# Performance work log

Measured on AMD Instinct MI355X. Metric: run time of the kernel, lower is better.

The kernel has to match this reference:

```python
import jax, jax.numpy as jnp
import numpy as np

N_NODES = 100000
N_EDGES = 1600000
NUM_FEATURES = 128
HIDDEN = 128


def _linear_init(key, fan_in, fan_out):
    kw, kb = jax.random.split(key)
    bound = 1.0 / np.sqrt(fan_in)
    w = jax.random.uniform(kw, (fan_in, fan_out), jnp.float32, -bound, bound)
    b = jax.random.uniform(kb, (fan_out,), jnp.float32, -bound, bound)
    return w, b


def setup_inputs() -> dict:
    key = jax.random.key(0)
    ks = jax.random.split(key, 8)
    x = jax.random.normal(ks[0], (N_NODES, NUM_FEATURES), jnp.float32)
    edge_index = jax.random.randint(ks[1], (2, N_EDGES), 0, N_NODES, jnp.int64)
    w11, b11 = _linear_init(ks[2], NUM_FEATURES, HIDDEN)
    w12, b12 = _linear_init(ks[3], HIDDEN, HIDDEN)
    w21, b21 = _linear_init(ks[4], HIDDEN, HIDDEN)
    w22, b22 = _linear_init(ks[5], HIDDEN, HIDDEN)
    w31, b31 = _linear_init(ks[6], HIDDEN, HIDDEN)
    w32, b32 = _linear_init(ks[7], HIDDEN, 1)
    return {"x": x, "edge_index": edge_index,
            "w11": w11, "b11": b11, "w12": w12, "b12": b12,
            "w21": w21, "b21": b21, "w22": w22, "b22": b22,
            "w31": w31, "b31": b31, "w32": w32, "b32": b32}


def _gin_conv(x, src, dst, w1, b1, w2, b2):
    # GINConv (eps=0): h_i = MLP(x_i + sum_{j->i} x_j)
    agg = jax.ops.segment_sum(x[src], dst, num_segments=N_NODES)
    h = x + agg
    h = jax.nn.relu(h @ w1 + b1)
    return h @ w2 + b2


def reference(x, edge_index, w11, b11, w12, b12, w21, b21, w22, b22, w31, b31, w32, b32):
    src, dst = edge_index[0], edge_index[1]
    h = _gin_conv(x, src, dst, w11, b11, w12, b12)
    h = _gin_conv(h, src, dst, w21, b21, w22, b22)
    h = _gin_conv(h, src, dst, w31, b31, w32, b32)  # [N, 1]
    return h
```

## Files before the change

### kernel.cpp

```cpp
#include <hip/hip_runtime.h>

#define NN 100000
#define NE 1600000
#define F 128
#define NBUCK ((NN + 255) >> 8)
#define EPB (NE / 256)

typedef _Float16 f16x8 __attribute__((ext_vector_type(8)));
typedef float    f32x4 __attribute__((ext_vector_type(4)));
typedef unsigned short ushort8v __attribute__((ext_vector_type(8)));
typedef unsigned short ushort4v __attribute__((ext_vector_type(4)));

__device__ inline unsigned short f2h(float f) {
    _Float16 h = (_Float16)f;
    return __builtin_bit_cast(unsigned short, h);
}
__device__ inline float h2f(unsigned short u) {
    return (float)__builtin_bit_cast(_Float16, u);
}

__global__ __launch_bounds__(256) void k_bhist(const int* __restrict__ dst, int* __restrict__ bcnt) {
    __shared__ int sc[NBUCK];
    for (int i = threadIdx.x; i < NBUCK; i += 256) sc[i] = 0;
    __syncthreads();
    int stride = gridDim.x * 256;
    for (int e = blockIdx.x * 256 + threadIdx.x; e < NE; e += stride)
        atomicAdd(&sc[dst[e] >> 8], 1);
    __syncthreads();
    for (int i = threadIdx.x; i < NBUCK; i += 256) {
        int c = sc[i];
        if (c) atomicAdd(&bcnt[i], c);
    }
}

__global__ void k_bscan(const int* __restrict__ bcnt, int* __restrict__ bbase, int* __restrict__ bcur) {
    __shared__ int s[512];
    int t = threadIdx.x;
    int v = (t < NBUCK) ? bcnt[t] : 0;
    s[t] = v;
    __syncthreads();
    for (int off = 1; off < 512; off <<= 1) {
        int u = (t >= off) ? s[t - off] : 0;
        __syncthreads();
        s[t] += u;
        __syncthreads();
    }
    int excl = s[t] - v;
    if (t < NBUCK) { bbase[t] = excl; bcur[t] = excl; }
    if (t == 0) bbase[NBUCK] = NE;
}

__global__ __launch_bounds__(256) void k_scatterA(const int* __restrict__ src,
                                                  const int* __restrict__ dst,
                                                  int* __restrict__ bcur,
                                                  unsigned* __restrict__ scratch) {
    __shared__ uint2 sEdge[EPB];
    __shared__ int cnt[512];
    __shared__ int scn[512];
    __shared__ int cntB[512];
    __shared__ int gbase[512];
    __shared__ int ssum[256];

    const int tid = threadIdx.x;
    const int ebase = blockIdx.x * EPB;

#pragma unroll
    for (int i = tid; i < 512; i += 256) { cnt[i] = 0; cntB[i] = 0; }
    __syncthreads();

    for (int i = tid; i < EPB; i += 256) {
        int b = dst[ebase + i] >> 8;
        atomicAdd(&cnt[b], 1);
    }
    __syncthreads();

    int c0 = cnt[2 * tid], c1 = cnt[2 * tid + 1];
    ssum[tid] = c0 + c1;
    __syncthreads();
    for (int off = 1; off < 256; off <<= 1) {
        int v = (tid >= off) ? ssum[tid - off] : 0;
        __syncthreads();
        ssum[tid] += v;
        __syncthreads();
    }
    int texcl = (tid == 0) ? 0 : ssum[tid - 1];
    scn[2 * tid] = texcl;
    scn[2 * tid + 1] = texcl + c0;
#pragma unroll
    for (int i = tid; i < NBUCK; i += 256) {
        int c = cnt[i];
        gbase[i] = c ? atomicAdd(&bcur[i], c) : 0;
    }
    __syncthreads();

    for (int i = tid; i < EPB; i += 256) {
        int s = src[ebase + i], d = dst[ebase + i];
        int b = d >> 8;
        int rank = atomicAdd(&cntB[b], 1);
        sEdge[scn[b] + rank] = make_uint2((unsigned)s, (unsigned)d);
    }
    __syncthreads();

    for (int i = tid; i < EPB; i += 256) {
        uint2 ed = sEdge[i];
        int b = (int)(ed.y >> 8);
        unsigned w = ((ed.y & 255u) << 24) | ed.x;
        scratch[gbase[b] + (i - scn[b])] = w;
    }
}

__global__ __launch_bounds__(256) void k_fillB(const int* __restrict__ bbase,
                                               const unsigned* __restrict__ scratch,
                                               int* __restrict__ row_ptr,
                                               int* __restrict__ csr) {
    __shared__ int cnt[256];
    __shared__ int s[256];
    __shared__ int cur[256];
    int b = blockIdx.x;
    int base = bbase[b], end = bbase[b + 1];
    int t = threadIdx.x;
    cnt[t] = 0;
    __syncthreads();
    for (int i = base + t; i < end; i += 256)
        atomicAdd(&cnt[scratch[i] >> 24], 1);
    __syncthreads();
    int v = cnt[t];
    s[t] = v;
    __syncthreads();
    for (int off = 1; off < 256; off <<= 1) {
        int u = (t >= off) ? s[t - off] : 0;
        __syncthreads();
        s[t] += u;
        __syncthreads();
    }
    int excl = s[t] - v;
    int node = (b << 8) + t;
    if (node < NN) row_ptr[node] = base + excl;
    if (b == NBUCK - 1 && t == 0) row_ptr[NN] = NE;
    cur[t] = excl;
    __syncthreads();
    for (int i = base + t; i < end; i += 256) {
        unsigned w = scratch[i];
        int n = w >> 24;
        int p = atomicAdd(&cur[n], 1);
        csr[base + p] = (int)(w & 0xFFFFFFu);
    }
}

__global__ void k_x2h(const float* __restrict__ x, unsigned short* __restrict__ xh) {
    int idx = blockIdx.x * 256 + threadIdx.x;
    float4 v = ((const float4*)x)[idx];
    ushort4v h;
    h.x = f2h(v.x);
    h.y = f2h(v.y);
    h.z = f2h(v.z);
    h.w = f2h(v.w);
    ((ushort4v*)xh)[idx] = h;
}

struct WPack {
    const float* w[5];
    unsigned short* t[5];
};

__global__ void k_w2h(WPack p) {
    int which = blockIdx.x >> 6;
    int idx = (blockIdx.x & 63) * 256 + threadIdx.x;
    int n = idx >> 7, k = idx & 127;
    p.t[which][idx] = f2h(p.w[which][k * 128 + n]);
}

__global__ __launch_bounds__(256) void k_agg(const unsigned short* __restrict__ h,
                                             const int* __restrict__ row_ptr,
                                             const int* __restrict__ csr,
                                             unsigned short* __restrict__ u) {
    int g   = threadIdx.x >> 4;
    int l16 = threadIdx.x & 15;
    int node = blockIdx.x * 16 + g;
    int lofs = l16 * 8;
    size_t base = (size_t)node * F + lofs;
    ushort8v sh = *(const ushort8v*)&h[base];
    float a[8];
#pragma unroll
    for (int k = 0; k < 8; ++k) a[k] = h2f(sh[k]);
    int s = row_ptr[node], e = row_ptr[node + 1];
    int p = s;
    for (; p + 8 <= e; p += 8) {
        ushort8v v[8];
#pragma unroll
        for (int q = 0; q < 8; ++q) {
            int j = csr[p + q];
            v[q] = *(const ushort8v*)&h[(size_t)j * F + lofs];
        }
#pragma unroll
        for (int k = 0; k < 8; ++k) {
            float t0 = (h2f(v[0][k]) + h2f(v[1][k])) + (h2f(v[2][k]) + h2f(v[3][k]));
            float t1 = (h2f(v[4][k]) + h2f(v[5][k])) + (h2f(v[6][k]) + h2f(v[7][k]));
            a[k] += t0 + t1;
        }
    }
    if (p + 4 <= e) {
        ushort8v v[4];
#pragma unroll
        for (int q = 0; q < 4; ++q) {
            int j = csr[p + q];
            v[q] = *(const ushort8v*)&h[(size_t)j * F + lofs];
        }
#pragma unroll
        for (int k = 0; k < 8; ++k)
            a[k] += (h2f(v[0][k]) + h2f(v[1][k])) + (h2f(v[2][k]) + h2f(v[3][k]));
        p += 4;
    }
    if (p + 2 <= e) {
        int j0 = csr[p], j1 = csr[p + 1];
        ushort8v v0 = *(const ushort8v*)&h[(size_t)j0 * F + lofs];
        ushort8v v1 = *(const ushort8v*)&h[(size_t)j1 * F + lofs];
#pragma unroll
        for (int k = 0; k < 8; ++k) a[k] += h2f(v0[k]) + h2f(v1[k]);
        p += 2;
    }
    if (p < e) {
        int j0 = csr[p];
        ushort8v v0 = *(const ushort8v*)&h[(size_t)j0 * F + lofs];
#pragma unroll
        for (int k = 0; k < 8; ++k) a[k] += h2f(v0[k]);
    }
    ushort8v o;
#pragma unroll
    for (int k = 0; k < 8; ++k) o[k] = f2h(a[k]);
    *(ushort8v*)&u[base] = o;
}

template <int L3>
__global__ __launch_bounds__(256, 6) void k_mlp(const unsigned short* __restrict__ A,
                                                const unsigned short* __restrict__ W1,
                                                const float* __restrict__ b1,
                                                const unsigned short* __restrict__ W2,
                                                const float* __restrict__ b2,
                                                const float* __restrict__ w32,
                                                const float* __restrict__ b32,
                                                unsigned short* __restrict__ H,
                                                float* __restrict__ out) {
    __shared__ __align__(16) unsigned short sA[64 * 128];

    const int tid = threadIdx.x;
    const int row0 = blockIdx.x * 64;
    const int cg   = tid >> 6;
    const int lane = tid & 63;
    const int m16  = lane & 15;
    const int quad = lane >> 4;

    {
        const ushort8v* g = (const ushort8v*)(A + (size_t)row0 * F);
#pragma unroll
        for (int i = 0; i < 4; ++i) {
            int fg = i * 256 + tid;
            int r = fg >> 4, u = fg & 15;
            ushort8v v = {};
            if (row0 + r < NN) v = g[fg];
            *(ushort8v*)&sA[r * 128 + ((u ^ (r & 15)) << 3)] = v;
        }
    }
    __syncthreads();

    f32x4 acc[4][2] = {};
#pragma unroll
    for (int ks = 0; ks < 4; ++ks) {
        f16x8 a[4];
#pragma unroll
        for (int rt = 0; rt < 4; ++rt) {
            int rowL = rt * 16 + m16;
            int u = ks * 4 + quad;
            a[rt] = *(const f16x8*)&sA[rowL * 128 + ((u ^ (rowL & 15)) << 3)];
        }
#pragma unroll
        for (int ct = 0; ct < 2; ++ct) {
            int widx = (cg * 32 + ct * 16 + m16) * 128 + ks * 32 + quad * 8;
            f16x8 b = *(const f16x8*)&W1[widx];
#pragma unroll
            for (int rt = 0; rt < 4; ++rt)
                acc[rt][ct] = __builtin_amdgcn_mfma_f32_16x16x32_f16(a[rt], b, acc[rt][ct], 0, 0, 0);
        }
    }

    if (L3) {
        float* psf = (float*)sA;
        __syncthreads();
#pragma unroll
        for (int rt = 0; rt < 4; ++rt) {
            float s[4] = {0.f, 0.f, 0.f, 0.f};
#pragma unroll
            for (int ct = 0; ct < 2; ++ct) {
                int col = cg * 32 + ct * 16 + m16;
                float bv = b1[col];
                float wv = w32[col];
#pragma unroll
                for (int i = 0; i < 4; ++i) {
                    float v = fmaxf(acc[rt][ct][i] + bv, 0.f);
                    s[i] += v * wv;
                }
            }
#pragma unroll
            for (int i = 0; i < 4; ++i) {
#pragma unroll
                for (int mask = 1; mask < 16; mask <<= 1)
                    s[i] += __shfl_xor(s[i], mask, 64);
            }
            if (m16 == 0) {
#pragma unroll
                for (int i = 0; i < 4; ++i) {
                    int rowL = rt * 16 + quad * 4 + i;
                    psf[rowL * 4 + cg] = s[i];
                }
            }
        }
        __syncthreads();
        if (tid < 64) {
            int row = row0 + tid;
            if (row < NN)
                out[row] = (psf[tid * 4] + psf[tid * 4 + 1]) + (psf[tid * 4 + 2] + psf[tid * 4 + 3]) + b32[0];
        }
        return;
    }

    __syncthreads();
#pragma unroll
    for (int rt = 0; rt < 4; ++rt) {
#pragma unroll
        for (int ct = 0; ct < 2; ++ct) {
            int col = cg * 32 + ct * 16 + m16;
            float bv = b1[col];
#pragma unroll
            for (int i = 0; i < 4; ++i) {
                int rL = rt * 16 + quad * 4 + i;
                float v = fmaxf(acc[rt][ct][i] + bv, 0.f);
                sA[rL * 128 + (((col >> 3) ^ (rL & 15)) << 3) + (col & 7)] = f2h(v);
            }
        }
    }
    __syncthreads();

    f32x4 acc2[4][2] = {};
#pragma unroll
    for (int ks = 0; ks < 4; ++ks) {
        f16x8 a[4];
#pragma unroll
        for (int rt = 0; rt < 4; ++rt) {
            int rowL = rt * 16 + m16;
            int u = ks * 4 + quad;
            a[rt] = *(const f16x8*)&sA[rowL * 128 + ((u ^ (rowL & 15)) << 3)];
        }
#pragma unroll
        for (int ct = 0; ct < 2; ++ct) {
            int widx = (cg * 32 + ct * 16 + m16) * 128 + ks * 32 + quad * 8;
            f16x8 b = *(const f16x8*)&W2[widx];
#pragma unroll
            for (int rt = 0; rt < 4; ++rt)
                acc2[rt][ct] = __builtin_amdgcn_mfma_f32_16x16x32_f16(a[rt], b, acc2[rt][ct], 0, 0, 0);
        }
    }

    __syncthreads();
#pragma unroll
    for (int rt = 0; rt < 4; ++rt) {
#pragma unroll
        for (int ct = 0; ct < 2; ++ct) {
            int col = cg * 32 + ct * 16 + m16;
            float bv = b2[col];
#pragma unroll
            for (int i = 0; i < 4; ++i) {
                int rL = rt * 16 + quad * 4 + i;
                float v = acc2[rt][ct][i] + bv;
                sA[rL * 128 + (((col >> 3) ^ (rL & 15)) << 3) + (col & 7)] = f2h(v);
            }
        }
    }
    __syncthreads();
    {
        ushort8v* go = (ushort8v*)(H + (size_t)row0 * F);
#pragma unroll
        for (int i = 0; i < 4; ++i) {
            int fg = i * 256 + tid;
            int r = fg >> 4, u = fg & 15;
            if (row0 + r < NN)
                go[fg] = *(const ushort8v*)&sA[r * 128 + ((u ^ (r & 15)) << 3)];
        }
    }
}

static inline size_t align256(size_t x) { return (x + 255) & ~(size_t)255; }

extern "C" void kernel_launch(void* const* d_in, const int* in_sizes, int n_in,
                              void* d_out, int out_size, void* d_ws, size_t ws_size,
                              hipStream_t stream) {
    const float* x   = (const float*)d_in[0];
    const int*   ei  = (const int*)d_in[1];
    const float* w11 = (const float*)d_in[2];
    const float* b11 = (const float*)d_in[3];
    const float* w12 = (const float*)d_in[4];
    const float* b12 = (const float*)d_in[5];
    const float* w21 = (const float*)d_in[6];
    const float* b21 = (const float*)d_in[7];
    const float* w22 = (const float*)d_in[8];
    const float* b22 = (const float*)d_in[9];
    const float* w31 = (const float*)d_in[10];
    const float* b31 = (const float*)d_in[11];
    const float* w32 = (const float*)d_in[12];
    const float* b32 = (const float*)d_in[13];
    float* out = (float*)d_out;

    const int* src = ei;
    const int* dst = ei + NE;

    char* ws = (char*)d_ws;
    size_t off = 0;
    unsigned short* Abuf = (unsigned short*)(ws + off); off += align256((size_t)NN * F * 2);
    unsigned short* Bbuf = (unsigned short*)(ws + off); off += align256((size_t)NN * F * 2);
    int* bcnt    = (int*)(ws + off); off += align256((size_t)NBUCK * 4);
    int* bbase   = (int*)(ws + off); off += align256((size_t)(NBUCK + 1) * 4);
    int* bcur    = (int*)(ws + off); off += align256((size_t)NBUCK * 4);
    int* row_ptr = (int*)(ws + off); off += align256((size_t)(NN + 1) * 4);
    int* csr     = (int*)(ws + off); off += align256((size_t)NE * 4);
    unsigned* scratch = (unsigned*)(ws + off); off += align256((size_t)NE * 4);
    unsigned short* wt[5];
    for (int i = 0; i < 5; ++i) {
        wt[i] = (unsigned short*)(ws + off); off += align256((size_t)128 * 128 * 2);
    }
    (void)ws_size;

    WPack wp;
    wp.w[0] = w11; wp.w[1] = w12; wp.w[2] = w21; wp.w[3] = w22; wp.w[4] = w31;
    for (int i = 0; i < 5; ++i) wp.t[i] = wt[i];
    k_w2h<<<320, 256, 0, stream>>>(wp);
    k_x2h<<<(NN * F / 4 + 255) / 256, 256, 0, stream>>>(x, Abuf);

    (void)hipMemsetAsync(bcnt, 0, (size_t)NBUCK * 4, stream);
    k_bhist<<<256, 256, 0, stream>>>(dst, bcnt);
    k_bscan<<<1, 512, 0, stream>>>(bcnt, bbase, bcur);
    k_scatterA<<<256, 256, 0, stream>>>(src, dst, bcur, scratch);
    k_fillB<<<NBUCK, 256, 0, stream>>>(bbase, scratch, row_ptr, csr);

    const int aggBlocks = NN / 16;
    const int mlpBlocks = (NN + 63) / 64;

    k_agg<<<aggBlocks, 256, 0, stream>>>(Abuf, row_ptr, csr, Bbuf);
    k_mlp<0><<<mlpBlocks, 256, 0, stream>>>(Bbuf, wt[0], b11, wt[1], b12,
                                            nullptr, nullptr, Abuf, nullptr);
    k_agg<<<aggBlocks, 256, 0, stream>>>(Abuf, row_ptr, csr, Bbuf);
    k_mlp<0><<<mlpBlocks, 256, 0, stream>>>(Bbuf, wt[2], b21, wt[3], b22,
                                            nullptr, nullptr, Abuf, nullptr);
    k_agg<<<aggBlocks, 256, 0, stream>>>(Abuf, row_ptr, csr, Bbuf);
    k_mlp<1><<<mlpBlocks, 256, 0, stream>>>(Bbuf, wt[4], b31, nullptr, nullptr,
                                            w32, b32, nullptr, out);
}
```

Baseline: 442.2 us.

## Slice node features into 8 column planes for cache-local aggregation

Stores the fp16 feature matrices as 8 planes of 16 columns each (32 bytes per node per plane) instead of row-major 256-byte rows. Aggregation blocks each work on one plane for 128 nodes, so the gather working set per plane (about 3.2 MB) can stay resident in L2/LLC while random neighbor rows are fetched. The conversion and MLP load/store paths are rewritten to read and write the planar layout. The cost is smaller 32-byte gather segments per edge and more strided MLP loads and stores.

```diff
diff --git a/kernel.cpp b/kernel.cpp
--- a/kernel.cpp
+++ b/kernel.cpp
@@ -5,6 +5,7 @@
 #define F 128
 #define NBUCK ((NN + 255) >> 8)
 #define EPB (NE / 256)
+#define PL ((size_t)NN * 16)
 
 typedef _Float16 f16x8 __attribute__((ext_vector_type(8)));
 typedef float    f32x4 __attribute__((ext_vector_type(4)));
@@ -148,14 +149,15 @@
 }
 
 __global__ void k_x2h(const float* __restrict__ x, unsigned short* __restrict__ xh) {
-    int idx = blockIdx.x * 256 + threadIdx.x;
-    float4 v = ((const float4*)x)[idx];
-    ushort4v h;
-    h.x = f2h(v.x);
-    h.y = f2h(v.y);
-    h.z = f2h(v.z);
-    h.w = f2h(v.w);
-    ((ushort4v*)xh)[idx] = h;
+    int i = blockIdx.x * 256 + threadIdx.x;
+    int n = i >> 4, g = i & 15;
+    int s = g >> 1, hh = g & 1;
+    const float4* src = (const float4*)(x + (size_t)n * F + g * 8);
+    float4 v0 = src[0], v1 = src[1];
+    ushort8v o;
+    o[0] = f2h(v0.x); o[1] = f2h(v0.y); o[2] = f2h(v0.z); o[3] = f2h(v0.w);
+    o[4] = f2h(v1.x); o[5] = f2h(v1.y); o[6] = f2h(v1.z); o[7] = f2h(v1.w);
+    *(ushort8v*)&xh[(size_t)s * PL + (size_t)n * 16 + hh * 8] = o;
 }
 
 struct WPack {
@@ -174,23 +176,28 @@
                                              const int* __restrict__ row_ptr,
                                              const int* __restrict__ csr,
                                              unsigned short* __restrict__ u) {
-    int g   = threadIdx.x >> 4;
-    int l16 = threadIdx.x & 15;
-    int node = blockIdx.x * 16 + g;
-    int lofs = l16 * 8;
-    size_t base = (size_t)node * F + lofs;
-    ushort8v sh = *(const ushort8v*)&h[base];
+    const int s  = blockIdx.x & 7;
+    const int nb = blockIdx.x >> 3;
+    const int rl = threadIdx.x >> 1;
+    const int hh = threadIdx.x & 1;
+    const int node = nb * 128 + rl;
+    if (node >= NN) return;
+    const unsigned short* P = h + (size_t)s * PL;
+    unsigned short* Q = u + (size_t)s * PL;
+    const size_t base = (size_t)node * 16 + hh * 8;
+    ushort8v sh = *(const ushort8v*)&P[base];
     float a[8];
 #pragma unroll
     for (int k = 0; k < 8; ++k) a[k] = h2f(sh[k]);
-    int s = row_ptr[node], e = row_ptr[node + 1];
-    int p = s;
+    int st = row_ptr[node], e = row_ptr[node + 1];
+    int p = st;
+    const int ho = hh * 8;
     for (; p + 8 <= e; p += 8) {
         ushort8v v[8];
 #pragma unroll
         for (int q = 0; q < 8; ++q) {
             int j = csr[p + q];
-            v[q] = *(const ushort8v*)&h[(size_t)j * F + lofs];
+            v[q] = *(const ushort8v*)&P[(size_t)j * 16 + ho];
         }
 #pragma unroll
         for (int k = 0; k < 8; ++k) {
@@ -204,7 +211,7 @@
 #pragma unroll
         for (int q = 0; q < 4; ++q) {
             int j = csr[p + q];
-            v[q] = *(const ushort8v*)&h[(size_t)j * F + lofs];
+            v[q] = *(const ushort8v*)&P[(size_t)j * 16 + ho];
         }
 #pragma unroll
         for (int k = 0; k < 8; ++k)
@@ -213,22 +220,22 @@
     }
     if (p + 2 <= e) {
         int j0 = csr[p], j1 = csr[p + 1];
-        ushort8v v0 = *(const ushort8v*)&h[(size_t)j0 * F + lofs];
-        ushort8v v1 = *(const ushort8v*)&h[(size_t)j1 * F + lofs];
+        ushort8v v0 = *(const ushort8v*)&P[(size_t)j0 * 16 + ho];
+        ushort8v v1 = *(const ushort8v*)&P[(size_t)j1 * 16 + ho];
 #pragma unroll
         for (int k = 0; k < 8; ++k) a[k] += h2f(v0[k]) + h2f(v1[k]);
         p += 2;
     }
     if (p < e) {
         int j0 = csr[p];
-        ushort8v v0 = *(const ushort8v*)&h[(size_t)j0 * F + lofs];
+        ushort8v v0 = *(const ushort8v*)&P[(size_t)j0 * 16 + ho];
 #pragma unroll
         for (int k = 0; k < 8; ++k) a[k] += h2f(v0[k]);
     }
     ushort8v o;
 #pragma unroll
     for (int k = 0; k < 8; ++k) o[k] = f2h(a[k]);
-    *(ushort8v*)&u[base] = o;
+    *(ushort8v*)&Q[base] = o;
 }
 
 template <int L3>
@@ -250,16 +257,20 @@
     const int m16  = lane & 15;
     const int quad = lane >> 4;
 
-    {
-        const ushort8v* g = (const ushort8v*)(A + (size_t)row0 * F);
-#pragma unroll
-        for (int i = 0; i < 4; ++i) {
-            int fg = i * 256 + tid;
-            int r = fg >> 4, u = fg & 15;
-            ushort8v v = {};
-            if (row0 + r < NN) v = g[fg];
-            *(ushort8v*)&sA[r * 128 + ((u ^ (r & 15)) << 3)] = v;
-        }
+#pragma unroll
+    for (int it = 0; it < 2; ++it) {
+        int unit = it * 256 + tid;
+        int s = unit >> 6, r = unit & 63;
+        int node = row0 + r;
+        ushort8v v0 = {}, v1 = {};
+        if (node < NN) {
+            const unsigned short* P = A + (size_t)s * PL + (size_t)node * 16;
+            v0 = *(const ushort8v*)&P[0];
+            v1 = *(const ushort8v*)&P[8];
+        }
+        int u0 = 2 * s, u1 = 2 * s + 1;
+        *(ushort8v*)&sA[r * 128 + ((u0 ^ (r & 15)) << 3)] = v0;
+        *(ushort8v*)&sA[r * 128 + ((u1 ^ (r & 15)) << 3)] = v1;
     }
     __syncthreads();
 
@@ -376,14 +387,18 @@
         }
     }
     __syncthreads();
-    {
-        ushort8v* go = (ushort8v*)(H + (size_t)row0 * F);
-#pragma unroll
-        for (int i = 0; i < 4; ++i) {
-            int fg = i * 256 + tid;
-            int r = fg >> 4, u = fg & 15;
-            if (row0 + r < NN)
-                go[fg] = *(const ushort8v*)&sA[r * 128 + ((u ^ (r & 15)) << 3)];
+#pragma unroll
+    for (int it = 0; it < 2; ++it) {
+        int unit = it * 256 + tid;
+        int s = unit >> 6, r = unit & 63;
+        int node = row0 + r;
+        if (node < NN) {
+            int u0 = 2 * s, u1 = 2 * s + 1;
+            ushort8v v0 = *(const ushort8v*)&sA[r * 128 + ((u0 ^ (r & 15)) << 3)];
+            ushort8v v1 = *(const ushort8v*)&sA[r * 128 + ((u1 ^ (r & 15)) << 3)];
+            unsigned short* P = H + (size_t)s * PL + (size_t)node * 16;
+            *(ushort8v*)&P[0] = v0;
+            *(ushort8v*)&P[8] = v1;
         }
     }
 }
@@ -432,7 +447,7 @@
     wp.w[0] = w11; wp.w[1] = w12; wp.w[2] = w21; wp.w[3] = w22; wp.w[4] = w31;
     for (int i = 0; i < 5; ++i) wp.t[i] = wt[i];
     k_w2h<<<320, 256, 0, stream>>>(wp);
-    k_x2h<<<(NN * F / 4 + 255) / 256, 256, 0, stream>>>(x, Abuf);
+    k_x2h<<<NN * 16 / 256, 256, 0, stream>>>(x, Abuf);
 
     (void)hipMemsetAsync(bcnt, 0, (size_t)NBUCK * 4, stream);
     k_bhist<<<256, 256, 0, stream>>>(dst, bcnt);
@@ -440,7 +455,7 @@
     k_scatterA<<<256, 256, 0, stream>>>(src, dst, bcur, scratch);
     k_fillB<<<NBUCK, 256, 0, stream>>>(bbase, scratch, row_ptr, csr);
 
-    const int aggBlocks = NN / 16;
+    const int aggBlocks = ((NN + 127) / 128) * 8;
     const int mlpBlocks = (NN + 63) / 64;
 
     k_agg<<<aggBlocks, 256, 0, stream>>>(Abuf, row_ptr, csr, Bbuf);
```

Measured after the change: 491.1 us. +11.1%, slower.

## Fuse neighbor aggregation into MLP kernel, writing aggregates straight to LDS

Applied to the files above, without the earlier changes.

Merges the separate CSR gather-sum kernel into the per-layer MLP kernel, so each 64-row block aggregates its nodes' neighbors and writes the fp16 sums directly into the swizzled LDS tile. This removes the intermediate aggregate buffer's global write and read, plus one launch per layer. The fused kernel has lower occupancy (launch bounds 6 to 5), and a latency-bound gather now shares a block with the MFMA stage, which may reduce overlap. Ping-pong buffers are used because the gather reads the input while other blocks write the output.

```diff
diff --git a/kernel.cpp b/kernel.cpp
--- a/kernel.cpp
+++ b/kernel.cpp
@@ -170,77 +170,18 @@
     p.t[which][idx] = f2h(p.w[which][k * 128 + n]);
 }
 
-__global__ __launch_bounds__(256) void k_agg(const unsigned short* __restrict__ h,
-                                             const int* __restrict__ row_ptr,
-                                             const int* __restrict__ csr,
-                                             unsigned short* __restrict__ u) {
-    int g   = threadIdx.x >> 4;
-    int l16 = threadIdx.x & 15;
-    int node = blockIdx.x * 16 + g;
-    int lofs = l16 * 8;
-    size_t base = (size_t)node * F + lofs;
-    ushort8v sh = *(const ushort8v*)&h[base];
-    float a[8];
-#pragma unroll
-    for (int k = 0; k < 8; ++k) a[k] = h2f(sh[k]);
-    int s = row_ptr[node], e = row_ptr[node + 1];
-    int p = s;
-    for (; p + 8 <= e; p += 8) {
-        ushort8v v[8];
-#pragma unroll
-        for (int q = 0; q < 8; ++q) {
-            int j = csr[p + q];
-            v[q] = *(const ushort8v*)&h[(size_t)j * F + lofs];
-        }
-#pragma unroll
-        for (int k = 0; k < 8; ++k) {
-            float t0 = (h2f(v[0][k]) + h2f(v[1][k])) + (h2f(v[2][k]) + h2f(v[3][k]));
-            float t1 = (h2f(v[4][k]) + h2f(v[5][k])) + (h2f(v[6][k]) + h2f(v[7][k]));
-            a[k] += t0 + t1;
-        }
-    }
-    if (p + 4 <= e) {
-        ushort8v v[4];
-#pragma unroll
-        for (int q = 0; q < 4; ++q) {
-            int j = csr[p + q];
-            v[q] = *(const ushort8v*)&h[(size_t)j * F + lofs];
-        }
-#pragma unroll
-        for (int k = 0; k < 8; ++k)
-            a[k] += (h2f(v[0][k]) + h2f(v[1][k])) + (h2f(v[2][k]) + h2f(v[3][k]));
-        p += 4;
-    }
-    if (p + 2 <= e) {
-        int j0 = csr[p], j1 = csr[p + 1];
-        ushort8v v0 = *(const ushort8v*)&h[(size_t)j0 * F + lofs];
-        ushort8v v1 = *(const ushort8v*)&h[(size_t)j1 * F + lofs];
-#pragma unroll
-        for (int k = 0; k < 8; ++k) a[k] += h2f(v0[k]) + h2f(v1[k]);
-        p += 2;
-    }
-    if (p < e) {
-        int j0 = csr[p];
-        ushort8v v0 = *(const ushort8v*)&h[(size_t)j0 * F + lofs];
-#pragma unroll
-        for (int k = 0; k < 8; ++k) a[k] += h2f(v0[k]);
-    }
-    ushort8v o;
-#pragma unroll
-    for (int k = 0; k < 8; ++k) o[k] = f2h(a[k]);
-    *(ushort8v*)&u[base] = o;
-}
-
 template <int L3>
-__global__ __launch_bounds__(256, 6) void k_mlp(const unsigned short* __restrict__ A,
-                                                const unsigned short* __restrict__ W1,
-                                                const float* __restrict__ b1,
-                                                const unsigned short* __restrict__ W2,
-                                                const float* __restrict__ b2,
-                                                const float* __restrict__ w32,
-                                                const float* __restrict__ b32,
-                                                unsigned short* __restrict__ H,
-                                                float* __restrict__ out) {
+__global__ __launch_bounds__(256, 5) void k_layer(const unsigned short* __restrict__ G,
+                                                  const int* __restrict__ row_ptr,
+                                                  const int* __restrict__ csr,
+                                                  const unsigned short* __restrict__ W1,
+                                                  const float* __restrict__ b1,
+                                                  const unsigned short* __restrict__ W2,
+                                                  const float* __restrict__ b2,
+                                                  const float* __restrict__ w32,
+                                                  const float* __restrict__ b32,
+                                                  unsigned short* __restrict__ H,
+                                                  float* __restrict__ out) {
     __shared__ __align__(16) unsigned short sA[64 * 128];
 
     const int tid = threadIdx.x;
@@ -251,14 +192,65 @@
     const int quad = lane >> 4;
 
     {
-        const ushort8v* g = (const ushort8v*)(A + (size_t)row0 * F);
-#pragma unroll
-        for (int i = 0; i < 4; ++i) {
-            int fg = i * 256 + tid;
-            int r = fg >> 4, u = fg & 15;
-            ushort8v v = {};
-            if (row0 + r < NN) v = g[fg];
-            *(ushort8v*)&sA[r * 128 + ((u ^ (r & 15)) << 3)] = v;
+        const int g = tid >> 4;
+        const int l16 = tid & 15;
+        const int lofs = l16 * 8;
+#pragma unroll
+        for (int it = 0; it < 4; ++it) {
+            int r = it * 16 + g;
+            int node = row0 + r;
+            float a[8] = {};
+            if (node < NN) {
+                ushort8v sh = *(const ushort8v*)&G[(size_t)node * F + lofs];
+#pragma unroll
+                for (int k = 0; k < 8; ++k) a[k] = h2f(sh[k]);
+                int st = row_ptr[node], e = row_ptr[node + 1];
+                int p = st;
+                for (; p + 8 <= e; p += 8) {
+                    ushort8v v[8];
+#pragma unroll
+                    for (int q = 0; q < 8; ++q) {
+                        int j = csr[p + q];
+                        v[q] = *(const ushort8v*)&G[(size_t)j * F + lofs];
+                    }
+#pragma unroll
+                    for (int k = 0; k < 8; ++k) {
+                        float t0 = (h2f(v[0][k]) + h2f(v[1][k])) + (h2f(v[2][k]) + h2f(v[3][k]));
+                        float t1 = (h2f(v[4][k]) + h2f(v[5][k])) + (h2f(v[6][k]) + h2f(v[7][k]));
+                        a[k] += t0 + t1;
+                    }
+                }
+                if (p + 4 <= e) {
+                    ushort8v v[4];
+#pragma unroll
+                    for (int q = 0; q < 4; ++q) {
+                        int j = csr[p + q];
+                        v[q] = *(const ushort8v*)&G[(size_t)j * F + lofs];
+                    }
+#pragma unroll
+                    for (int k = 0; k < 8; ++k)
+                        a[k] += (h2f(v[0][k]) + h2f(v[1][k])) + (h2f(v[2][k]) + h2f(v[3][k]));
+                    p += 4;
+                }
+                if (p + 2 <= e) {
+                    int j0 = csr[p], j1 = csr[p + 1];
+                    ushort8v v0 = *(const ushort8v*)&G[(size_t)j0 * F + lofs];
+                    ushort8v v1 = *(const ushort8v*)&G[(size_t)j1 * F + lofs];
+#pragma unroll
+                    for (int k = 0; k < 8; ++k) a[k] += h2f(v0[k]) + h2f(v1[k]);
+                    p += 2;
+                }
+                if (p < e) {
+                    int j0 = csr[p];
+                    ushort8v v0 = *(const ushort8v*)&G[(size_t)j0 * F + lofs];
+#pragma unroll
+                    for (int k = 0; k < 8; ++k) a[k] += h2f(v0[k]);
+                }
+            }
+            ushort8v o;
+#pragma unroll
+            for (int k = 0; k < 8; ++k) o[k] = f2h(a[k]);
+            *(ushort8v*)&sA[r * 128 + ((l16 ^ (r & 15)) << 3)] = o;
         }
     }
     __syncthreads();
@@ -440,16 +432,15 @@
     k_scatterA<<<256, 256, 0, stream>>>(src, dst, bcur, scratch);
     k_fillB<<<NBUCK, 256, 0, stream>>>(bbase, scratch, row_ptr, csr);
 
-    const int aggBlocks = NN / 16;
-    const int mlpBlocks = (NN + 63) / 64;
-
-    k_agg<<<aggBlocks, 256, 0, stream>>>(Abuf, row_ptr, csr, Bbuf);
-    k_mlp<0><<<mlpBlocks, 256, 0, stream>>>(Bbuf, wt[0], b11, wt[1], b12,
-                                            nullptr, nullptr, Abuf, nullptr);
-    k_agg<<<aggBlocks, 256, 0, stream>>>(Abuf, row_ptr, csr, Bbuf);
-    k_mlp<0><<<mlpBlocks, 256, 0, stream>>>(Bbuf, wt[2], b21, wt[3], b22,
-                                            nullptr, nullptr, Abuf, nullptr);
-    k_agg<<<aggBlocks, 256, 0, stream>>>(Abuf, row_ptr, csr, Bbuf);
-    k_mlp<1><<<mlpBlocks, 256, 0, stream>>>(Bbuf, wt[4], b31, nullptr, nullptr,
-                                            w32, b32, nullptr, out);
-}
+    const int layerBlocks = (NN + 63) / 64;
+
+    k_layer<0><<<layerBlocks, 256, 0, stream>>>(Abuf, row_ptr, csr,
+                                                wt[0], b11, wt[1], b12,
+                                                nullptr, nullptr, Bbuf, nullptr);
+    k_layer<0><<<layerBlocks, 256, 0, stream>>>(Bbuf, row_ptr, csr,
+                                                wt[2], b21, wt[3], b22,
+                                                nullptr, nullptr, Abuf, nullptr);
+    k_layer<1><<<layerBlocks, 256, 0, stream>>>(Abuf, row_ptr, csr,
+                                                wt[4], b31, nullptr, nullptr,
+                                                w32, b32, nullptr, out);
+}
```

Result: faster. 412.3 us (-6.8%).
